# Kernel tuning notes

Hardware: AMD Instinct MI355X
Metric: run time of the kernel (lower is better)

Reference implementation:

```python
import jax, jax.numpy as jnp
import numpy as np

B, S, D = 4, 4096, 1024


def setup_inputs() -> dict:
    key = jax.random.key(0)
    ks = jax.random.split(key, 4)
    scale = 1.0 / np.sqrt(D)
    x = jax.random.normal(ks[0], (B, S, D), dtype=jnp.float32)
    Wg = jax.random.normal(ks[1], (D, D), dtype=jnp.float32) * scale
    Wv = jax.random.normal(ks[2], (D, D), dtype=jnp.float32) * scale
    Wd = jax.random.normal(ks[3], (D, D), dtype=jnp.float32) * scale
    bg = jnp.zeros((D,), dtype=jnp.float32)
    bv = jnp.zeros((D,), dtype=jnp.float32)
    bd = jnp.ones((D,), dtype=jnp.float32)  # decay_bias_init = 1.0
    return {"x": x, "Wg": Wg, "bg": bg, "Wv": Wv, "bv": bv, "Wd": Wd, "bd": bd}


def _scan_causal(x_scan, a):
    # h_t = a_t * h_{t-1} + x_t, scanned over time; x_scan, a: [B,S,D]
    def step(h, inp):
        a_t, x_t = inp
        h = a_t * h + x_t
        return h, h

    h0 = jnp.zeros(x_scan.shape[::2], dtype=x_scan.dtype)  # [B,D]
    xs = (jnp.swapaxes(a, 0, 1), jnp.swapaxes(x_scan, 0, 1))  # [S,B,D]
    _, out = jax.lax.scan(step, h0, xs)
    return jnp.swapaxes(out, 0, 1)  # back to [B,S,D]


def reference(x, Wg, bg, Wv, bv, Wd, bd):
    # nn.Linear: y = x @ W.T + b
    g = jnp.einsum('bsd,ed->bse', x, Wg) + bg
    v = jnp.einsum('bsd,ed->bse', x, Wv) + bv
    d = jnp.einsum('bsd,ed->bse', x, Wd) + bd
    x_scan = jax.nn.sigmoid(g) * jnp.tanh(v)
    a = 0.001 + 0.998 * jax.nn.sigmoid(d)
    return _scan_causal(x_scan, a)
```

## Files before the change

### kernel.cpp

```cpp
#include <hip/hip_runtime.h>
#include <cstddef>
#include <cstdint>


typedef _Float16 f16;
typedef f16 f16x4 __attribute__((ext_vector_type(4)));
typedef f16 f16x8 __attribute__((ext_vector_type(8)));
typedef float f32x4 __attribute__((ext_vector_type(4)));

#define S_LEN 4096
#define D_DIM 1024
#define B_DIM 4
#define M_TOT (B_DIM * S_LEN)
#define N_TOT (3 * D_DIM)
#define K_TOT D_DIM

#define CHUNKS 128
#define CLEN (S_LEN / CHUNKS)

__global__ void cvt_f16_kernel(const float* __restrict__ src, f16* __restrict__ dst, int n) {
  int i = (blockIdx.x * blockDim.x + threadIdx.x) * 8;
  if (i >= n) return;
  f32x4 a = *(const f32x4*)(src + i);
  f32x4 b = *(const f32x4*)(src + i + 4);
  f16x8 o;
  o[0] = (f16)a[0]; o[1] = (f16)a[1]; o[2] = (f16)a[2]; o[3] = (f16)a[3];
  o[4] = (f16)b[0]; o[5] = (f16)b[1]; o[6] = (f16)b[2]; o[7] = (f16)b[3];
  *(f16x8*)(dst + i) = o;
}

#define BM 128
#define BN 128
#define BK 32

__device__ __forceinline__ void gl_lds16(const void* g, void* l) {
  __builtin_amdgcn_global_load_lds((const __attribute__((address_space(1))) void*)g,
                                   (__attribute__((address_space(3))) void*)l, 16, 0, 0);
}

__global__ __launch_bounds__(256) void gemm_f16_kernel(const f16* __restrict__ A,
                                                       const f16* __restrict__ Bt,
                                                       f16* __restrict__ C) {
  __shared__ __attribute__((aligned(16))) f16 As[BM * BK];
  __shared__ __attribute__((aligned(16))) f16 Bs[BN * BK];
  const int tid = threadIdx.x;
  const int lane = tid & 63;
  const int wave = tid >> 6;
  const int m0 = blockIdx.y * BM;
  const int n0 = blockIdx.x * BN;

  const int srow = tid >> 2;
  const int scol = (tid & 3) * 8;
  const f16* aG0 = A + (size_t)(m0 + srow) * K_TOT + scol;
  const f16* aG1 = A + (size_t)(m0 + srow + 64) * K_TOT + scol;
  const f16* bG0 = Bt + (size_t)(n0 + srow) * K_TOT + scol;
  const f16* bG1 = Bt + (size_t)(n0 + srow + 64) * K_TOT + scol;
  f16* aL0 = &As[tid * 8];
  f16* aL1 = &As[2048 + tid * 8];
  f16* bL0 = &Bs[tid * 8];
  f16* bL1 = &Bs[2048 + tid * 8];

  const int wm = (wave >> 1) * 64;
  const int wn = (wave & 1) * 64;
  const int lm = lane & 15;
  const int kq = (lane >> 4) * 8;

  f32x4 acc[4][4] = {};

  for (int k0 = 0; k0 < K_TOT; k0 += BK) {
    gl_lds16(aG0 + k0, aL0);
    gl_lds16(aG1 + k0, aL1);
    gl_lds16(bG0 + k0, bL0);
    gl_lds16(bG1 + k0, bL1);
    __syncthreads();
    f16x8 af[4], bf[4];
#pragma unroll
    for (int i = 0; i < 4; ++i)
      af[i] = *(const f16x8*)&As[(wm + i * 16 + lm) * BK + kq];
#pragma unroll
    for (int j = 0; j < 4; ++j)
      bf[j] = *(const f16x8*)&Bs[(wn + j * 16 + lm) * BK + kq];
#pragma unroll
    for (int i = 0; i < 4; ++i)
#pragma unroll
      for (int j = 0; j < 4; ++j)
        acc[i][j] = __builtin_amdgcn_mfma_f32_16x16x32_f16(af[i], bf[j], acc[i][j], 0, 0, 0);
    __syncthreads();
  }

  const int cm = m0 + wm + (lane >> 4) * 4;
  const int cn = n0 + wn + (lane & 15);
#pragma unroll
  for (int i = 0; i < 4; ++i)
#pragma unroll
    for (int j = 0; j < 4; ++j)
#pragma unroll
      for (int r = 0; r < 4; ++r)
        C[(size_t)(cm + i * 16 + r) * N_TOT + (cn + j * 16)] = (f16)acc[i][j][r];
}

__global__ void scan1_kernel(const f16* __restrict__ G, const float* __restrict__ bg,
                             const float* __restrict__ bv, const float* __restrict__ bd,
                             f16* __restrict__ xsA, f16* __restrict__ aA,
                             float* __restrict__ P, float* __restrict__ H) {
  const int u = blockIdx.x * 256 + threadIdx.x;
  const int cg = u & 255;
  const int b = (u >> 8) & 3;
  const int ck = u >> 10;
  const int ch = cg * 4;
  const f32x4 vbg = *(const f32x4*)(bg + ch);
  const f32x4 vbv = *(const f32x4*)(bv + ch);
  const f32x4 vbd = *(const f32x4*)(bd + ch);
  f32x4 h = {0.f, 0.f, 0.f, 0.f};
  f32x4 p = {1.f, 1.f, 1.f, 1.f};
  const int t0 = ck * CLEN;
#pragma unroll 4
  for (int t = t0; t < t0 + CLEN; ++t) {
    const size_t m = (size_t)b * S_LEN + t;
    const f16* gp = G + m * N_TOT + ch;
    f16x4 g4 = *(const f16x4*)gp;
    f16x4 v4 = *(const f16x4*)(gp + D_DIM);
    f16x4 d4 = *(const f16x4*)(gp + 2 * D_DIM);
    f16x4 xs4, a4;
#pragma unroll
    for (int j = 0; j < 4; ++j) {
      float gg = (float)g4[j] + vbg[j];
      float vv = (float)v4[j] + vbv[j];
      float dd = (float)d4[j] + vbd[j];
      float sg = 1.f / (1.f + __expf(-gg));
      float tv = 1.f - 2.f / (__expf(2.f * vv) + 1.f);
      float sd = 1.f / (1.f + __expf(-dd));
      f16 xh = (f16)(sg * tv);
      f16 ah = (f16)(0.001f + 0.998f * sd);
      float xsr = (float)xh, avr = (float)ah;
      h[j] = avr * h[j] + xsr;
      p[j] *= avr;
      xs4[j] = xh;
      a4[j] = ah;
    }
    *(f16x4*)(xsA + m * D_DIM + ch) = xs4;
    *(f16x4*)(aA + m * D_DIM + ch) = a4;
  }
  const int idx = ck * 4096 + b * D_DIM + ch;
  *(f32x4*)(P + idx) = p;
  *(f32x4*)(H + idx) = h;
}

__global__ void scan2_kernel(const float* __restrict__ P, const float* __restrict__ H,
                             float* __restrict__ carry) {
  const int idx = blockIdx.x * 256 + threadIdx.x;
  float h = 0.f;
  for (int c = 0; c < CHUNKS; ++c) {
    carry[c * 4096 + idx] = h;
    h = P[c * 4096 + idx] * h + H[c * 4096 + idx];
  }
}

__global__ void scan3_kernel(const f16* __restrict__ xsA, const f16* __restrict__ aA,
                             const float* __restrict__ carry, float* __restrict__ out) {
  const int u = blockIdx.x * 256 + threadIdx.x;
  const int cg = u & 255;
  const int b = (u >> 8) & 3;
  const int ck = u >> 10;
  const int ch = cg * 4;
  f32x4 h = *(const f32x4*)(carry + ck * 4096 + b * D_DIM + ch);
  const int t0 = ck * CLEN;
#pragma unroll 4
  for (int t = t0; t < t0 + CLEN; ++t) {
    const size_t m = (size_t)b * S_LEN + t;
    f16x4 xs4 = *(const f16x4*)(xsA + m * D_DIM + ch);
    f16x4 a4 = *(const f16x4*)(aA + m * D_DIM + ch);
#pragma unroll
    for (int j = 0; j < 4; ++j) h[j] = (float)a4[j] * h[j] + (float)xs4[j];
    *(f32x4*)(out + m * D_DIM + ch) = h;
  }
}

extern "C" void kernel_launch(void* const* d_in, const int* in_sizes, int n_in,
                              void* d_out, int out_size, void* d_ws, size_t ws_size,
                              hipStream_t stream) {
  const float* x = (const float*)d_in[0];
  const float* Wg = (const float*)d_in[1];
  const float* bg = (const float*)d_in[2];
  const float* Wv = (const float*)d_in[3];
  const float* bv = (const float*)d_in[4];
  const float* Wd = (const float*)d_in[5];
  const float* bd = (const float*)d_in[6];
  float* out = (float*)d_out;

  char* ws = (char*)d_ws;
  f16* Ah = (f16*)(ws);
  f16* Bh = (f16*)(ws + 33554432);
  f16* Gh = (f16*)(ws + 39845888);
  f16* xsA = (f16*)(ws + 140509184);
  f16* aA = (f16*)(ws + 174063616);
  float* P = (float*)(ws + 207618048);
  float* H = (float*)(ws + 209715200);
  float* carry = (float*)(ws + 211812352);

  cvt_f16_kernel<<<8192, 256, 0, stream>>>(x, Ah, M_TOT * K_TOT);
  cvt_f16_kernel<<<512, 256, 0, stream>>>(Wg, Bh, D_DIM * D_DIM);
  cvt_f16_kernel<<<512, 256, 0, stream>>>(Wv, Bh + D_DIM * D_DIM, D_DIM * D_DIM);
  cvt_f16_kernel<<<512, 256, 0, stream>>>(Wd, Bh + 2 * D_DIM * D_DIM, D_DIM * D_DIM);
  gemm_f16_kernel<<<dim3(N_TOT / BN, M_TOT / BM), 256, 0, stream>>>(Ah, Bh, Gh);
  scan1_kernel<<<512, 256, 0, stream>>>(Gh, bg, bv, bd, xsA, aA, P, H);
  scan2_kernel<<<16, 256, 0, stream>>>(P, H, carry);
  scan3_kernel<<<512, 256, 0, stream>>>(xsA, aA, carry, out);
}
```

Measured before the change: 338.5 us.

## Merge conversion kernels, stage GEMM output through LDS, widen scan vectors

The four fp32-to-fp16 conversion launches become one kernel. The GEMM epilogue now writes the tile to padded LDS and then stores coalesced 16-byte rows instead of scattered 2-byte stores. The scan kernels process 8 channels per thread with 16-byte accesses. Chunks shrink to 16 steps with a per-batch chunk layout, which makes the serial carry pass 256 long. P, H and carry reuse the A buffer, which is dead once the GEMM finishes. The longer serial scan2 loop may cost more than it saves.

Result: no change. 338.2 us (-0.1%).

```diff
diff --git a/kernel.cpp b/kernel.cpp
--- a/kernel.cpp
+++ b/kernel.cpp
@@ -4,7 +4,6 @@
 
 
 typedef _Float16 f16;
-typedef f16 f16x4 __attribute__((ext_vector_type(4)));
 typedef f16 f16x8 __attribute__((ext_vector_type(8)));
 typedef float f32x4 __attribute__((ext_vector_type(4)));
 
@@ -15,23 +14,38 @@
 #define N_TOT (3 * D_DIM)
 #define K_TOT D_DIM
 
-#define CHUNKS 128
-#define CLEN (S_LEN / CHUNKS)
-
-__global__ void cvt_f16_kernel(const float* __restrict__ src, f16* __restrict__ dst, int n) {
-  int i = (blockIdx.x * blockDim.x + threadIdx.x) * 8;
-  if (i >= n) return;
-  f32x4 a = *(const f32x4*)(src + i);
-  f32x4 b = *(const f32x4*)(src + i + 4);
+#define CLEN 16
+#define CPB (S_LEN / CLEN)
+#define NCHUNK (B_DIM * CPB)
+
+__device__ __forceinline__ void cvt8(const float* s, f16* d) {
+  f32x4 a = *(const f32x4*)s;
+  f32x4 b = *(const f32x4*)(s + 4);
   f16x8 o;
   o[0] = (f16)a[0]; o[1] = (f16)a[1]; o[2] = (f16)a[2]; o[3] = (f16)a[3];
   o[4] = (f16)b[0]; o[5] = (f16)b[1]; o[6] = (f16)b[2]; o[7] = (f16)b[3];
-  *(f16x8*)(dst + i) = o;
+  *(f16x8*)d = o;
+}
+
+__global__ void cvt_all_kernel(const float* __restrict__ x, const float* __restrict__ w0,
+                               const float* __restrict__ w1, const float* __restrict__ w2,
+                               f16* __restrict__ Ah, f16* __restrict__ Bh) {
+  int i = (blockIdx.x * 256 + threadIdx.x) * 8;
+  if (i < M_TOT * K_TOT) {
+    cvt8(x + i, Ah + i);
+  } else {
+    int w = i - M_TOT * K_TOT;
+    int sel = w >> 20;
+    int loc = w & 1048575;
+    const float* s = (sel == 0) ? w0 : (sel == 1) ? w1 : w2;
+    cvt8(s + loc, Bh + w);
+  }
 }
 
 #define BM 128
 #define BN 128
 #define BK 32
+#define CT_PITCH 136
 
 __device__ __forceinline__ void gl_lds16(const void* g, void* l) {
   __builtin_amdgcn_global_load_lds((const __attribute__((address_space(1))) void*)g,
@@ -41,8 +55,9 @@
 __global__ __launch_bounds__(256) void gemm_f16_kernel(const f16* __restrict__ A,
                                                        const f16* __restrict__ Bt,
                                                        f16* __restrict__ C) {
-  __shared__ __attribute__((aligned(16))) f16 As[BM * BK];
-  __shared__ __attribute__((aligned(16))) f16 Bs[BN * BK];
+  __shared__ __attribute__((aligned(16))) char smem[BM * CT_PITCH * 2];
+  f16* As = (f16*)smem;
+  f16* Bs = As + 4096;
   const int tid = threadIdx.x;
   const int lane = tid & 63;
   const int wave = tid >> 6;
@@ -55,10 +70,10 @@
   const f16* aG1 = A + (size_t)(m0 + srow + 64) * K_TOT + scol;
   const f16* bG0 = Bt + (size_t)(n0 + srow) * K_TOT + scol;
   const f16* bG1 = Bt + (size_t)(n0 + srow + 64) * K_TOT + scol;
-  f16* aL0 = &As[tid * 8];
-  f16* aL1 = &As[2048 + tid * 8];
-  f16* bL0 = &Bs[tid * 8];
-  f16* bL1 = &Bs[2048 + tid * 8];
+  f16* aL0 = As + tid * 8;
+  f16* aL1 = As + 2048 + tid * 8;
+  f16* bL0 = Bs + tid * 8;
+  f16* bL1 = Bs + 2048 + tid * 8;
 
   const int wm = (wave >> 1) * 64;
   const int wn = (wave & 1) * 64;
@@ -88,15 +103,24 @@
     __syncthreads();
   }
 
-  const int cm = m0 + wm + (lane >> 4) * 4;
-  const int cn = n0 + wn + (lane & 15);
+  f16* Ct = (f16*)smem;
+  const int r0 = wm + (lane >> 4) * 4;
+  const int c0 = wn + (lane & 15);
 #pragma unroll
   for (int i = 0; i < 4; ++i)
 #pragma unroll
     for (int j = 0; j < 4; ++j)
 #pragma unroll
       for (int r = 0; r < 4; ++r)
-        C[(size_t)(cm + i * 16 + r) * N_TOT + (cn + j * 16)] = (f16)acc[i][j][r];
+        Ct[(r0 + i * 16 + r) * CT_PITCH + c0 + j * 16] = (f16)acc[i][j][r];
+  __syncthreads();
+#pragma unroll
+  for (int p = 0; p < 8; ++p) {
+    int row = p * 16 + (tid >> 4);
+    int col = (tid & 15) * 8;
+    *(f16x8*)(C + (size_t)(m0 + row) * N_TOT + n0 + col) =
+        *(const f16x8*)&Ct[row * CT_PITCH + col];
+  }
 }
 
 __global__ void scan1_kernel(const f16* __restrict__ G, const float* __restrict__ bg,
@@ -104,29 +128,29 @@
                              f16* __restrict__ xsA, f16* __restrict__ aA,
                              float* __restrict__ P, float* __restrict__ H) {
   const int u = blockIdx.x * 256 + threadIdx.x;
-  const int cg = u & 255;
-  const int b = (u >> 8) & 3;
-  const int ck = u >> 10;
-  const int ch = cg * 4;
-  const f32x4 vbg = *(const f32x4*)(bg + ch);
-  const f32x4 vbv = *(const f32x4*)(bv + ch);
-  const f32x4 vbd = *(const f32x4*)(bd + ch);
-  f32x4 h = {0.f, 0.f, 0.f, 0.f};
-  f32x4 p = {1.f, 1.f, 1.f, 1.f};
+  const int cg = u & 127;
+  const int b = (u >> 7) & 3;
+  const int ck = u >> 9;
+  const int ch = cg * 8;
+  float vbg[8], vbv[8], vbd[8];
+  *(f32x4*)vbg = *(const f32x4*)(bg + ch); *(f32x4*)(vbg + 4) = *(const f32x4*)(bg + ch + 4);
+  *(f32x4*)vbv = *(const f32x4*)(bv + ch); *(f32x4*)(vbv + 4) = *(const f32x4*)(bv + ch + 4);
+  *(f32x4*)vbd = *(const f32x4*)(bd + ch); *(f32x4*)(vbd + 4) = *(const f32x4*)(bd + ch + 4);
+  float h[8] = {}, p[8] = {1.f, 1.f, 1.f, 1.f, 1.f, 1.f, 1.f, 1.f};
   const int t0 = ck * CLEN;
-#pragma unroll 4
+#pragma unroll 2
   for (int t = t0; t < t0 + CLEN; ++t) {
     const size_t m = (size_t)b * S_LEN + t;
     const f16* gp = G + m * N_TOT + ch;
-    f16x4 g4 = *(const f16x4*)gp;
-    f16x4 v4 = *(const f16x4*)(gp + D_DIM);
-    f16x4 d4 = *(const f16x4*)(gp + 2 * D_DIM);
-    f16x4 xs4, a4;
-#pragma unroll
-    for (int j = 0; j < 4; ++j) {
-      float gg = (float)g4[j] + vbg[j];
-      float vv = (float)v4[j] + vbv[j];
-      float dd = (float)d4[j] + vbd[j];
+    f16x8 g8 = *(const f16x8*)gp;
+    f16x8 v8 = *(const f16x8*)(gp + D_DIM);
+    f16x8 d8 = *(const f16x8*)(gp + 2 * D_DIM);
+    f16x8 xs8, a8;
+#pragma unroll
+    for (int j = 0; j < 8; ++j) {
+      float gg = (float)g8[j] + vbg[j];
+      float vv = (float)v8[j] + vbv[j];
+      float dd = (float)d8[j] + vbd[j];
       float sg = 1.f / (1.f + __expf(-gg));
       float tv = 1.f - 2.f / (__expf(2.f * vv) + 1.f);
       float sd = 1.f / (1.f + __expf(-dd));
@@ -135,44 +159,54 @@
       float xsr = (float)xh, avr = (float)ah;
       h[j] = avr * h[j] + xsr;
       p[j] *= avr;
-      xs4[j] = xh;
-      a4[j] = ah;
+      xs8[j] = xh;
+      a8[j] = ah;
     }
-    *(f16x4*)(xsA + m * D_DIM + ch) = xs4;
-    *(f16x4*)(aA + m * D_DIM + ch) = a4;
-  }
-  const int idx = ck * 4096 + b * D_DIM + ch;
-  *(f32x4*)(P + idx) = p;
-  *(f32x4*)(H + idx) = h;
+    *(f16x8*)(xsA + m * D_DIM + ch) = xs8;
+    *(f16x8*)(aA + m * D_DIM + ch) = a8;
+  }
+  const int base = (b * CPB + ck) * D_DIM + ch;
+  *(f32x4*)(P + base) = *(f32x4*)p;
+  *(f32x4*)(P + base + 4) = *(f32x4*)(p + 4);
+  *(f32x4*)(H + base) = *(f32x4*)h;
+  *(f32x4*)(H + base + 4) = *(f32x4*)(h + 4);
 }
 
 __global__ void scan2_kernel(const float* __restrict__ P, const float* __restrict__ H,
                              float* __restrict__ carry) {
   const int idx = blockIdx.x * 256 + threadIdx.x;
+  const int b = idx >> 10;
+  const int d = idx & 1023;
   float h = 0.f;
-  for (int c = 0; c < CHUNKS; ++c) {
-    carry[c * 4096 + idx] = h;
-    h = P[c * 4096 + idx] * h + H[c * 4096 + idx];
+  for (int c = 0; c < CPB; ++c) {
+    int gs = b * CPB + c;
+    carry[gs * D_DIM + d] = h;
+    h = P[gs * D_DIM + d] * h + H[gs * D_DIM + d];
   }
 }
 
 __global__ void scan3_kernel(const f16* __restrict__ xsA, const f16* __restrict__ aA,
                              const float* __restrict__ carry, float* __restrict__ out) {
   const int u = blockIdx.x * 256 + threadIdx.x;
-  const int cg = u & 255;
-  const int b = (u >> 8) & 3;
-  const int ck = u >> 10;
-  const int ch = cg * 4;
-  f32x4 h = *(const f32x4*)(carry + ck * 4096 + b * D_DIM + ch);
+  const int cg = u & 127;
+  const int b = (u >> 7) & 3;
+  const int ck = u >> 9;
+  const int ch = cg * 8;
+  const int base = (b * CPB + ck) * D_DIM + ch;
+  float h[8];
+  *(f32x4*)h = *(const f32x4*)(carry + base);
+  *(f32x4*)(h + 4) = *(const f32x4*)(carry + base + 4);
   const int t0 = ck * CLEN;
-#pragma unroll 4
+#pragma unroll 2
   for (int t = t0; t < t0 + CLEN; ++t) {
     const size_t m = (size_t)b * S_LEN + t;
-    f16x4 xs4 = *(const f16x4*)(xsA + m * D_DIM + ch);
-    f16x4 a4 = *(const f16x4*)(aA + m * D_DIM + ch);
-#pragma unroll
-    for (int j = 0; j < 4; ++j) h[j] = (float)a4[j] * h[j] + (float)xs4[j];
-    *(f32x4*)(out + m * D_DIM + ch) = h;
+    f16x8 xs8 = *(const f16x8*)(xsA + m * D_DIM + ch);
+    f16x8 a8 = *(const f16x8*)(aA + m * D_DIM + ch);
+#pragma unroll
+    for (int j = 0; j < 8; ++j) h[j] = (float)a8[j] * h[j] + (float)xs8[j];
+    float* op = out + m * D_DIM + ch;
+    *(f32x4*)op = *(f32x4*)h;
+    *(f32x4*)(op + 4) = *(f32x4*)(h + 4);
   }
 }
 
@@ -190,18 +224,15 @@
 
   char* ws = (char*)d_ws;
   f16* Ah = (f16*)(ws);
+  float* P = (float*)(ws);
+  float* H = (float*)(ws + 4194304);
+  float* carry = (float*)(ws + 8388608);
   f16* Bh = (f16*)(ws + 33554432);
   f16* Gh = (f16*)(ws + 39845888);
   f16* xsA = (f16*)(ws + 140509184);
   f16* aA = (f16*)(ws + 174063616);
-  float* P = (float*)(ws + 207618048);
-  float* H = (float*)(ws + 209715200);
-  float* carry = (float*)(ws + 211812352);
-
-  cvt_f16_kernel<<<8192, 256, 0, stream>>>(x, Ah, M_TOT * K_TOT);
-  cvt_f16_kernel<<<512, 256, 0, stream>>>(Wg, Bh, D_DIM * D_DIM);
-  cvt_f16_kernel<<<512, 256, 0, stream>>>(Wv, Bh + D_DIM * D_DIM, D_DIM * D_DIM);
-  cvt_f16_kernel<<<512, 256, 0, stream>>>(Wd, Bh + 2 * D_DIM * D_DIM, D_DIM * D_DIM);
+
+  cvt_all_kernel<<<9728, 256, 0, stream>>>(x, Wg, Wv, Wd, Ah, Bh);
   gemm_f16_kernel<<<dim3(N_TOT / BN, M_TOT / BM), 256, 0, stream>>>(Ah, Bh, Gh);
   scan1_kernel<<<512, 256, 0, stream>>>(Gh, bg, bv, bd, xsA, aA, P, H);
   scan2_kernel<<<16, 256, 0, stream>>>(P, H, carry);
```
